# Kernel tuning notes

Measured on AMD Instinct MI355X. Metric: run time of the kernel, lower is better.

## Reference

```python
import jax, jax.numpy as jnp
import numpy as np

H, N, CH = 256, 64, 1

def _r2c(x):
    return x[..., 0] + 1j * x[..., 1]

def setup_inputs() -> dict:
    key = jax.random.key(0)
    kA, kB, kC, kdt = jax.random.split(key, 4)
    # Build a Hurwitz A (skew-Hermitian - 0.5*I) so dA = (I-dt/2 A)^-1 (I+dt/2 A) has spectral radius < 1
    M = jax.random.normal(kA, (H, N, N, 2), dtype=jnp.float32) / np.float32(np.sqrt(N))
    Mc = _r2c(M)
    Ac = 0.5 * (Mc - jnp.conjugate(jnp.swapaxes(Mc, -1, -2))) - 0.5 * jnp.eye(N, dtype=Mc.dtype)
    A = jnp.stack([Ac.real, Ac.imag], axis=-1)  # (H,N,N,2)
    B = jax.random.normal(kB, (H, N, 2), dtype=jnp.float32)
    C = jax.random.normal(kC, (CH, H, N, 2), dtype=jnp.float32)
    # log_dt uniform in [log(1e-3), log(1e-1)], shape (H,1) per bilinear docstring
    log_dt = jax.random.uniform(kdt, (H, 1), dtype=jnp.float32,
                                minval=np.float32(np.log(1e-3)), maxval=np.float32(np.log(1e-1)))
    return {"A": A, "B": B, "C": C, "log_dt": log_dt, "L": 2048}

def _bilinear(dt, Ac, Bc):
    # dt: (H,1), Ac: (H,N,N) complex, Bc: (H,N) complex
    n = Ac.shape[-1]
    I = jnp.eye(n, dtype=Ac.dtype)
    half = (dt.astype(Ac.real.dtype) / 2)[:, None]  # (H,1,1)
    A_back = I - half * Ac
    A_fwd = I + half * Ac
    dB = dt.astype(Ac.dtype) * jnp.linalg.solve(A_back, Bc[..., None])[..., 0]  # (H,N)
    dA = jnp.linalg.solve(A_back, A_fwd)  # (H,N,N)
    return dA, dB

def _krylov(L, dA, dB):
    # x[..., l] = dA^l dB via squaring-doubling, matches S4 krylov math
    x = dB[..., None]  # (H,N,1)
    A_ = dA
    while x.shape[-1] < L:
        x = jnp.concatenate([x, jnp.einsum('hnm,hml->hnl', A_, x)], axis=-1)
        A_ = A_ @ A_
    return x[..., :L]

def reference(A, B, C, log_dt, L):
    Ac, Bc, Cc = _r2c(A), _r2c(B), _r2c(C)
    dt = jnp.exp(log_dt)  # (H,1)
    dA, dB = _bilinear(dt, Ac, Bc)
    x = _krylov(L, dA, dB)  # (H,N,L) complex
    # k[c,h,l] = sum_n C[c,h,n] * (dA^l dB)[h,n]; torch .float() on complex keeps real part
    k = jnp.einsum('chn,hnl->chl', Cc, x).real.astype(jnp.float32)
    return k
```

## Files before the change

kernel.cpp:

```cpp
#include <hip/hip_runtime.h>
#include <math.h>

#define NH   256
#define NN   64
#define LSEQ 2048
#define SDW  68
#define NTH  1024

typedef __attribute__((ext_vector_type(8))) short short8;
typedef __attribute__((ext_vector_type(4))) float float4_t;

#define MFMA(a,b,c) __builtin_amdgcn_mfma_f32_16x16x32_bf16((a),(b),(c),0,0,0)
#define PERM_HI 0x07060302u
#define PERM_LO 0x05040100u

static __device__ __forceinline__ unsigned pack2(float v) {
    unsigned hv = __float_as_uint(v) & 0xffff0000u;
    float lo = v - __uint_as_float(hv);
    return __builtin_amdgcn_perm(hv, __float_as_uint(lo), PERM_HI);
}
static __device__ __forceinline__ float unpack2(unsigned w) {
    return __uint_as_float(w & 0xffff0000u) + __uint_as_float(w << 16);
}

static __device__ __forceinline__ void frag_vals(const unsigned* e, short8& hi, short8& lo) {
    unsigned lb[8];
#pragma unroll
    for (int m = 0; m < 8; ++m) {
        unsigned hv = e[m] & 0xffff0000u;
        lb[m] = __float_as_uint(__uint_as_float(e[m]) - __uint_as_float(hv));
    }
    union { short8 s; unsigned u[4]; } H, L;
#pragma unroll
    for (int m = 0; m < 4; ++m) {
        H.u[m] = __builtin_amdgcn_perm(e[2*m+1],  e[2*m],  PERM_HI);
        L.u[m] = __builtin_amdgcn_perm(lb[2*m+1], lb[2*m], PERM_HI);
    }
    hi = H.s; lo = L.s;
}
static __device__ __forceinline__ void frag_f32(const float* p, short8& hi, short8& lo) {
    const uint4* q = (const uint4*)p;
    uint4 d0 = q[0], d1 = q[1];
    unsigned e[8] = {d0.x, d0.y, d0.z, d0.w, d1.x, d1.y, d1.z, d1.w};
    frag_vals(e, hi, lo);
}
static __device__ __forceinline__ void frag_packed(const unsigned* p, short8& hi, short8& lo) {
    const uint4* q = (const uint4*)p;
    uint4 d0 = q[0], d1 = q[1];
    unsigned e[8] = {d0.x, d0.y, d0.z, d0.w, d1.x, d1.y, d1.z, d1.w};
    union { short8 s; unsigned u[4]; } H, L;
#pragma unroll
    for (int m = 0; m < 4; ++m) {
        H.u[m] = __builtin_amdgcn_perm(e[2*m+1], e[2*m], PERM_HI);
        L.u[m] = __builtin_amdgcn_perm(e[2*m+1], e[2*m], PERM_LO);
    }
    hi = H.s; lo = L.s;
}
static __device__ __forceinline__ short8 neg8(short8 v) {
    union { short8 s; int i[4]; } u; u.s = v;
#pragma unroll
    for (int m = 0; m < 4; ++m) u.i[m] ^= 0x80008000;
    return u.s;
}

template<bool AP, bool BP, bool IMAG>
static __device__ __forceinline__ void cmm_tile(
    const void* Ar_, const void* Ai_, const void* Br_, const void* Bi_,
    int arow, int bcol, int fq, float4_t& accR, float4_t& accI)
{
#pragma unroll
    for (int ks = 0; ks < 2; ++ks) {
        const int k0 = ks*32 + fq*8;
        short8 Arh, Arl, Aih, Ail, Brh, Brl, Bih, Bil;
        if (AP) {
            frag_packed((const unsigned*)Ar_ + arow*SDW + k0, Arh, Arl);
            frag_packed((const unsigned*)Ai_ + arow*SDW + k0, Aih, Ail);
        } else {
            frag_f32((const float*)Ar_ + arow*SDW + k0, Arh, Arl);
            frag_f32((const float*)Ai_ + arow*SDW + k0, Aih, Ail);
        }
        if (BP) {
            frag_packed((const unsigned*)Br_ + bcol*SDW + k0, Brh, Brl);
            frag_packed((const unsigned*)Bi_ + bcol*SDW + k0, Bih, Bil);
        } else {
            frag_f32((const float*)Br_ + bcol*SDW + k0, Brh, Brl);
            frag_f32((const float*)Bi_ + bcol*SDW + k0, Bih, Bil);
        }
        short8 nAih = neg8(Aih), nAil = neg8(Ail);
        accR = MFMA(Arh, Brh, accR); accR = MFMA(Arh, Brl, accR); accR = MFMA(Arl, Brh, accR);
        accR = MFMA(nAih, Bih, accR); accR = MFMA(nAih, Bil, accR); accR = MFMA(nAil, Bih, accR);
        if (IMAG) {
            accI = MFMA(Arh, Bih, accI); accI = MFMA(Arh, Bil, accI); accI = MFMA(Arl, Bih, accI);
            accI = MFMA(Aih, Brh, accI); accI = MFMA(Aih, Brl, accI); accI = MFMA(Ail, Brh, accI);
        }
    }
}

__global__ __launch_bounds__(NTH, 4) void ssm_kernel(
    const float* __restrict__ Ag,
    const float* __restrict__ Bg,
    const float* __restrict__ Cg,
    const float* __restrict__ LogDt,
    float* __restrict__ outp)
{
    __shared__ __align__(16) unsigned char lds[122880];
    unsigned* XRr = (unsigned*)(lds +      0);
    unsigned* XRi = (unsigned*)(lds +  17408);
    unsigned* XTr = (unsigned*)(lds +  34816);
    unsigned* XTi = (unsigned*)(lds +  52224);
    float*    Xfr = (float*)(lds +  69632);
    float*    Xfi = (float*)(lds +  87040);
    unsigned* U0u = (unsigned*)Xfr;
    unsigned* U1u = (unsigned*)Xfi;
    float*    Grf = (float*)(lds + 104448);
    float*    Gif = (float*)(lds + 113152);
    float*    bvr = (float*)(lds + 121856);
    float*    bvi = (float*)(lds + 122112);
    float*    urr = (float*)(lds + 122368);
    float*    uri = (float*)(lds + 122624);

    const int t    = threadIdx.x;
    const int lane = t & 63;
    const int wv   = t >> 6;
    const int ti   = wv >> 2, tj = wv & 3;
    const int fm   = lane & 15, fq = lane >> 4;
    const int h    = blockIdx.x;

    const float dt  = expf(LogDt[h]);
    const float hdt = 0.5f * dt;

    const float2* A2 = (const float2*)(Ag + (size_t)h * NN * NN * 2);
    const float4_t z4 = {0.f, 0.f, 0.f, 0.f};

#pragma unroll
    for (int e = 0; e < 4; ++e) {
        int idx = t + e*NTH;
        int i = idx >> 6, j = idx & 63;
        float2 a = A2[idx];
        unsigned pr = pack2((i == j ? 1.0f : 0.0f) + hdt * a.x);
        unsigned pi = pack2(hdt * a.y);
        XRr[i*SDW + j] = pr; XRi[i*SDW + j] = pi;
        XTr[j*SDW + i] = pr; XTi[j*SDW + i] = pi;
    }
    if (t < NN) {
        float2 bv = ((const float2*)Bg)[h*NN + t];
        float2 cv = ((const float2*)Cg)[h*NN + t];
        bvr[t] = bv.x; bvi[t] = bv.y;
        Grf[t] = cv.x; Gif[t] = cv.y;
    }
    __syncthreads();

    const int arow = ti*16 + fm;
    const int bcol = tj*16 + fm;

    {
        float4_t aR = z4, aI = z4;
#pragma unroll
        for (int ks = 0; ks < 2; ++ks) {
            const int k0 = ks*32 + fq*8;
            unsigned vr[8], vi[8];
#pragma unroll
            for (int j = 0; j < 8; ++j) {
                float2 a = A2[arow*NN + k0 + j];
                vr[j] = __float_as_uint((arow == k0 + j ? 1.0f : 0.0f) - hdt * a.x);
                vi[j] = __float_as_uint(-hdt * a.y);
            }
            short8 Arh, Arl, Aih, Ail, Brh, Brl, Bih, Bil;
            frag_vals(vr, Arh, Arl);
            frag_vals(vi, Aih, Ail);
            frag_packed(XTr + bcol*SDW + k0, Brh, Brl);
            frag_packed(XTi + bcol*SDW + k0, Bih, Bil);
            short8 nAih = neg8(Aih), nAil = neg8(Ail);
            aR = MFMA(Arh, Brh, aR); aR = MFMA(Arh, Brl, aR); aR = MFMA(Arl, Brh, aR);
            aR = MFMA(nAih, Bih, aR); aR = MFMA(nAih, Bil, aR); aR = MFMA(nAil, Bih, aR);
            aI = MFMA(Arh, Bih, aI); aI = MFMA(Arh, Bil, aI); aI = MFMA(Arl, Bih, aI);
            aI = MFMA(Aih, Brh, aI); aI = MFMA(Aih, Brl, aI); aI = MFMA(Ail, Brh, aI);
        }
#pragma unroll
        for (int rp = 0; rp < 2; ++rp) {
            int row0 = ti*16 + fq*4 + rp*2;
            uint2 wr; wr.x = pack2(aR[rp*2]); wr.y = pack2(aR[rp*2+1]);
            uint2 wi; wi.x = pack2(aI[rp*2]); wi.y = pack2(aI[rp*2+1]);
            *(uint2*)(U0u + bcol*SDW + row0) = wr;
            *(uint2*)(U1u + bcol*SDW + row0) = wi;
        }
    }
    __syncthreads();

    {
        float4_t aR = z4, aI = z4;
        cmm_tile<true, true, true>(XRr, XRi, U0u, U1u, arow, bcol, fq, aR, aI);
        __syncthreads();
#pragma unroll
        for (int r = 0; r < 4; ++r) {
            int row = ti*16 + fq*4 + r;
            XRr[row*SDW + bcol] = pack2(aR[r]);
            XRi[row*SDW + bcol] = pack2(aI[r]);
        }
    }
    __syncthreads();

    {
        float4_t aR = z4, aI = z4;
        cmm_tile<true, true, true>(XRr, XRi, U0u, U1u, arow, bcol, fq, aR, aI);
        float p_r[4], p_i[4];
#pragma unroll
        for (int r = 0; r < 4; ++r) {
            int row = ti*16 + fq*4 + r;
            float2 a = A2[row*NN + bcol];
            float dd  = (row == bcol ? 1.0f : 0.0f);
            float x1r = dd + hdt * a.x;
            float x1i = hdt * a.y;
            float vvr = unpack2(XRr[row*SDW + bcol]);
            float vvi = unpack2(XRi[row*SDW + bcol]);
            p_r[r] = 2.0f*(3.0f*x1r - 3.0f*vvr + aR[r]) - dd;
            p_i[r] = 2.0f*(3.0f*x1i - 3.0f*vvi + aI[r]);
        }
        __syncthreads();
        unsigned pr[4], pi[4];
#pragma unroll
        for (int r = 0; r < 4; ++r) {
            int row = ti*16 + fq*4 + r;
            pr[r] = pack2(p_r[r]); pi[r] = pack2(p_i[r]);
            XRr[row*SDW + bcol] = pr[r]; XRi[row*SDW + bcol] = pi[r];
        }
#pragma unroll
        for (int rp = 0; rp < 2; ++rp) {
            int row0 = ti*16 + fq*4 + rp*2;
            uint2 wr; wr.x = pr[rp*2]; wr.y = pr[rp*2+1];
            uint2 wi; wi.x = pi[rp*2]; wi.y = pi[rp*2+1];
            *(uint2*)(XTr + bcol*SDW + row0) = wr;
            *(uint2*)(XTi + bcol*SDW + row0) = wi;
        }
    }
    __syncthreads();

    {
        int n = t >> 4, part = t & 15;
        float ar = 0.f, ai = 0.f;
#pragma unroll
        for (int qq = 0; qq < 4; ++qq) {
            int k = part + 16*qq;
            float mr = unpack2(XRr[n*SDW + k]), mi = unpack2(XRi[n*SDW + k]);
            ar += mr*bvr[k] - mi*bvi[k];
            ai += mr*bvi[k] + mi*bvr[k];
        }
#pragma unroll
        for (int off = 8; off; off >>= 1) { ar += __shfl_xor(ar, off); ai += __shfl_xor(ai, off); }
        if (part == 0) { urr[n] = ar; uri[n] = ai; }
    }
    __syncthreads();

#pragma unroll 1
    for (int s = 1; s <= 9; ++s) {
        if (s == 1) {
            int n = t >> 4, part = t & 15;
            float ar = 0.f, ai = 0.f;
#pragma unroll
            for (int qq = 0; qq < 4; ++qq) {
                int k = part + 16*qq;
                float mr = unpack2(XRr[n*SDW + k]), mi = unpack2(XRi[n*SDW + k]);
                ar += mr*urr[k] - mi*uri[k];
                ai += mr*uri[k] + mi*urr[k];
            }
#pragma unroll
            for (int off = 8; off; off >>= 1) { ar += __shfl_xor(ar, off); ai += __shfl_xor(ai, off); }
            if (part == 0) {
                float u_r = urr[n], u_i = uri[n];
                Xfr[n]       = hdt*(u_r + bvr[n]);
                Xfi[n]       = hdt*(u_i + bvi[n]);
                Xfr[SDW + n] = hdt*(ar + u_r);
                Xfi[SDW + n] = hdt*(ai + u_i);
            }
        } else if (s <= 6) {
            const int C = 1 << (s-1);
            const int nT = (s == 6) ? 8 : 4;
            if (wv < nT) {
                const int rt = wv >> 2, ct = wv & 3;
                float4_t aR = z4, aI = z4;
                cmm_tile<false, true, true>(Xfr, Xfi, XRr, XRi, rt*16 + fm, ct*16 + fm, fq, aR, aI);
#pragma unroll
                for (int r = 0; r < 4; ++r) {
                    int row = rt*16 + fq*4 + r;
                    Xfr[(C+row)*SDW + ct*16 + fm] = aR[r];
                    Xfi[(C+row)*SDW + ct*16 + fm] = aI[r];
                }
            }
        } else {
            const int C = 1 << (s-7);
            if (wv < 4) {
                float4_t aR = z4, aI = z4;
                cmm_tile<false, true, true>(Grf, Gif, XTr, XTi, fm, wv*16 + fm, fq, aR, aI);
#pragma unroll
                for (int r = 0; r < 4; ++r) {
                    int row = C + fq*4 + r;
                    Grf[row*SDW + wv*16 + fm] = aR[r];
                    Gif[row*SDW + wv*16 + fm] = aI[r];
                }
            }
        }
        float4_t sR = z4, sI = z4;
        cmm_tile<true, true, true>(XRr, XRi, XTr, XTi, arow, bcol, fq, sR, sI);
        __syncthreads();
        unsigned pr[4], pi[4];
#pragma unroll
        for (int r = 0; r < 4; ++r) {
            int row = ti*16 + fq*4 + r;
            pr[r] = pack2(sR[r]); pi[r] = pack2(sI[r]);
            XRr[row*SDW + bcol] = pr[r]; XRi[row*SDW + bcol] = pi[r];
        }
#pragma unroll
        for (int rp = 0; rp < 2; ++rp) {
            int row0 = ti*16 + fq*4 + rp*2;
            uint2 wr; wr.x = pr[rp*2]; wr.y = pr[rp*2+1];
            uint2 wi; wi.x = pi[rp*2]; wi.y = pi[rp*2+1];
            *(uint2*)(XTr + bcol*SDW + row0) = wr;
            *(uint2*)(XTi + bcol*SDW + row0) = wi;
        }
        __syncthreads();
    }

#pragma unroll 1
    for (int tt = 0; tt < 4; ++tt) {
        if (tt < 3 && wv < 4) {
            const int ab = tt * 8;
            float4_t aR = z4, aI = z4;
            cmm_tile<false, true, true>(Grf, Gif, XTr, XTi, ab + fm, wv*16 + fm, fq, aR, aI);
#pragma unroll
            for (int r = 0; r < 4; ++r) {
                int orow = 8 + ab + fq*4 + r;
                if (orow < 32) {
                    Grf[orow*SDW + wv*16 + fm] = aR[r];
                    Gif[orow*SDW + wv*16 + fm] = aI[r];
                }
            }
        }
        if (wv >= 4 && wv < 8) {
            const int jb = tt * 8;
            float4_t aR = z4, aI = z4;
            cmm_tile<false, false, false>(Grf, Gif, Xfr, Xfi, jb + fm, (wv-4)*16 + fm, fq, aR, aI);
            if (fq < 2) {
                size_t base = (size_t)h * LSEQ;
#pragma unroll
                for (int r = 0; r < 4; ++r)
                    outp[base + (jb + fq*4 + r)*NN + (wv-4)*16 + fm] = aR[r];
            }
        }
        if (tt < 3) __syncthreads();
    }
}

extern "C" void kernel_launch(void* const* d_in, const int* in_sizes, int n_in,
                              void* d_out, int out_size, void* d_ws, size_t ws_size,
                              hipStream_t stream) {
    const float* A  = (const float*)d_in[0];
    const float* B  = (const float*)d_in[1];
    const float* C  = (const float*)d_in[2];
    const float* ld = (const float*)d_in[3];
    float* out = (float*)d_out;
    ssm_kernel<<<dim3(NH), dim3(NTH), 0, stream>>>(A, B, C, ld, out);
}
```

Before: 96.55 us.

## Store matrices as pre-split bf16 hi/lo planes and split complex accumulators

Replaces the packed hi/lo-in-one-word and fp32 shared-memory layouts with four separate bf16 planes (real hi, real lo, imag hi, imag lo) per matrix. MFMA fragments then load directly as short8 vectors with no perm or split work in the inner loop. The negation of the imaginary operand is dropped by accumulating the two real-part products in separate registers and subtracting at the end, and the imaginary part likewise uses two accumulators. This costs more accumulator registers, more LDS (about 127 KB) and more scattered 16-bit stores when writing results, and the fp32 buffers are now also held as split bf16.

```diff
diff --git a/kernel.cpp b/kernel.cpp
--- a/kernel.cpp
+++ b/kernel.cpp
@@ -4,23 +4,25 @@
 #define NH   256
 #define NN   64
 #define LSEQ 2048
-#define SDW  68
+#define RS   72
+#define PSZ  4608
+#define GSZ  2304
 #define NTH  1024
 
 typedef __attribute__((ext_vector_type(8))) short short8;
 typedef __attribute__((ext_vector_type(4))) float float4_t;
+typedef unsigned short u16;
 
 #define MFMA(a,b,c) __builtin_amdgcn_mfma_f32_16x16x32_bf16((a),(b),(c),0,0,0)
 #define PERM_HI 0x07060302u
-#define PERM_LO 0x05040100u
-
-static __device__ __forceinline__ unsigned pack2(float v) {
-    unsigned hv = __float_as_uint(v) & 0xffff0000u;
-    float lo = v - __uint_as_float(hv);
-    return __builtin_amdgcn_perm(hv, __float_as_uint(lo), PERM_HI);
-}
-static __device__ __forceinline__ float unpack2(unsigned w) {
-    return __uint_as_float(w & 0xffff0000u) + __uint_as_float(w << 16);
+
+static __device__ __forceinline__ void split2(float v, unsigned& hb, unsigned& lb) {
+    hb = __float_as_uint(v) & 0xffff0000u;
+    lb = __float_as_uint(v - __uint_as_float(hb));
+}
+static __device__ __forceinline__ float ld2(const u16* hp, const u16* lp, int idx) {
+    return __uint_as_float((unsigned)hp[idx] << 16)
+         + __uint_as_float((unsigned)lp[idx] << 16);
 }
 
 static __device__ __forceinline__ void frag_vals(const unsigned* e, short8& hi, short8& lo) {
@@ -38,62 +40,64 @@
     }
     hi = H.s; lo = L.s;
 }
-static __device__ __forceinline__ void frag_f32(const float* p, short8& hi, short8& lo) {
-    const uint4* q = (const uint4*)p;
-    uint4 d0 = q[0], d1 = q[1];
-    unsigned e[8] = {d0.x, d0.y, d0.z, d0.w, d1.x, d1.y, d1.z, d1.w};
-    frag_vals(e, hi, lo);
-}
-static __device__ __forceinline__ void frag_packed(const unsigned* p, short8& hi, short8& lo) {
-    const uint4* q = (const uint4*)p;
-    uint4 d0 = q[0], d1 = q[1];
-    unsigned e[8] = {d0.x, d0.y, d0.z, d0.w, d1.x, d1.y, d1.z, d1.w};
-    union { short8 s; unsigned u[4]; } H, L;
-#pragma unroll
-    for (int m = 0; m < 4; ++m) {
-        H.u[m] = __builtin_amdgcn_perm(e[2*m+1], e[2*m], PERM_HI);
-        L.u[m] = __builtin_amdgcn_perm(e[2*m+1], e[2*m], PERM_LO);
-    }
-    hi = H.s; lo = L.s;
-}
-static __device__ __forceinline__ short8 neg8(short8 v) {
-    union { short8 s; int i[4]; } u; u.s = v;
-#pragma unroll
-    for (int m = 0; m < 4; ++m) u.i[m] ^= 0x80008000;
-    return u.s;
-}
-
-template<bool AP, bool BP, bool IMAG>
+
+template<int ASZ, int BSZ, bool IMAG>
 static __device__ __forceinline__ void cmm_tile(
-    const void* Ar_, const void* Ai_, const void* Br_, const void* Bi_,
-    int arow, int bcol, int fq, float4_t& accR, float4_t& accI)
+    const u16* __restrict__ Ab, const u16* __restrict__ Bb,
+    int arow, int bcol, int fq,
+    float4_t& accP, float4_t& accN, float4_t& accI1, float4_t& accI2)
 {
 #pragma unroll
     for (int ks = 0; ks < 2; ++ks) {
         const int k0 = ks*32 + fq*8;
-        short8 Arh, Arl, Aih, Ail, Brh, Brl, Bih, Bil;
-        if (AP) {
-            frag_packed((const unsigned*)Ar_ + arow*SDW + k0, Arh, Arl);
-            frag_packed((const unsigned*)Ai_ + arow*SDW + k0, Aih, Ail);
-        } else {
-            frag_f32((const float*)Ar_ + arow*SDW + k0, Arh, Arl);
-            frag_f32((const float*)Ai_ + arow*SDW + k0, Aih, Ail);
-        }
-        if (BP) {
-            frag_packed((const unsigned*)Br_ + bcol*SDW + k0, Brh, Brl);
-            frag_packed((const unsigned*)Bi_ + bcol*SDW + k0, Bih, Bil);
-        } else {
-            frag_f32((const float*)Br_ + bcol*SDW + k0, Brh, Brl);
-            frag_f32((const float*)Bi_ + bcol*SDW + k0, Bih, Bil);
-        }
-        short8 nAih = neg8(Aih), nAil = neg8(Ail);
-        accR = MFMA(Arh, Brh, accR); accR = MFMA(Arh, Brl, accR); accR = MFMA(Arl, Brh, accR);
-        accR = MFMA(nAih, Bih, accR); accR = MFMA(nAih, Bil, accR); accR = MFMA(nAil, Bih, accR);
+        const u16* ap = Ab + arow*RS + k0;
+        const u16* bp = Bb + bcol*RS + k0;
+        short8 Arh = *(const short8*)(ap);
+        short8 Arl = *(const short8*)(ap + ASZ);
+        short8 Aih = *(const short8*)(ap + 2*ASZ);
+        short8 Ail = *(const short8*)(ap + 3*ASZ);
+        short8 Brh = *(const short8*)(bp);
+        short8 Brl = *(const short8*)(bp + BSZ);
+        short8 Bih = *(const short8*)(bp + 2*BSZ);
+        short8 Bil = *(const short8*)(bp + 3*BSZ);
+        accP = MFMA(Arh, Brh, accP); accP = MFMA(Arh, Brl, accP); accP = MFMA(Arl, Brh, accP);
+        accN = MFMA(Aih, Bih, accN); accN = MFMA(Aih, Bil, accN); accN = MFMA(Ail, Bih, accN);
         if (IMAG) {
-            accI = MFMA(Arh, Bih, accI); accI = MFMA(Arh, Bil, accI); accI = MFMA(Arl, Bih, accI);
-            accI = MFMA(Aih, Brh, accI); accI = MFMA(Aih, Brl, accI); accI = MFMA(Ail, Brh, accI);
-        }
-    }
+            accI1 = MFMA(Arh, Bih, accI1); accI1 = MFMA(Arh, Bil, accI1); accI1 = MFMA(Arl, Bih, accI1);
+            accI2 = MFMA(Aih, Brh, accI2); accI2 = MFMA(Aih, Brl, accI2); accI2 = MFMA(Ail, Brh, accI2);
+        }
+    }
+}
+
+static __device__ __forceinline__ void store_P_vals(
+    u16* XR, u16* XT, int ti, int bcol, int fq,
+    const float* p_r, const float* p_i)
+{
+    unsigned hR[4], lR[4], hI[4], lI[4];
+#pragma unroll
+    for (int r = 0; r < 4; ++r) {
+        split2(p_r[r], hR[r], lR[r]);
+        split2(p_i[r], hI[r], lI[r]);
+        int row = ti*16 + fq*4 + r;
+        XR[row*RS + bcol]         = (u16)(hR[r] >> 16);
+        XR[PSZ + row*RS + bcol]   = (u16)(lR[r] >> 16);
+        XR[2*PSZ + row*RS + bcol] = (u16)(hI[r] >> 16);
+        XR[3*PSZ + row*RS + bcol] = (u16)(lI[r] >> 16);
+    }
+    int tb = bcol*RS + ti*16 + fq*4;
+    uint2 w;
+    w.x = __builtin_amdgcn_perm(hR[1], hR[0], PERM_HI);
+    w.y = __builtin_amdgcn_perm(hR[3], hR[2], PERM_HI);
+    *(uint2*)&XT[tb] = w;
+    w.x = __builtin_amdgcn_perm(lR[1], lR[0], PERM_HI);
+    w.y = __builtin_amdgcn_perm(lR[3], lR[2], PERM_HI);
+    *(uint2*)&XT[PSZ + tb] = w;
+    w.x = __builtin_amdgcn_perm(hI[1], hI[0], PERM_HI);
+    w.y = __builtin_amdgcn_perm(hI[3], hI[2], PERM_HI);
+    *(uint2*)&XT[2*PSZ + tb] = w;
+    w.x = __builtin_amdgcn_perm(lI[1], lI[0], PERM_HI);
+    w.y = __builtin_amdgcn_perm(lI[3], lI[2], PERM_HI);
+    *(uint2*)&XT[3*PSZ + tb] = w;
 }
 
 __global__ __launch_bounds__(NTH, 4) void ssm_kernel(
@@ -103,21 +107,15 @@
     const float* __restrict__ LogDt,
     float* __restrict__ outp)
 {
-    __shared__ __align__(16) unsigned char lds[122880];
-    unsigned* XRr = (unsigned*)(lds +      0);
-    unsigned* XRi = (unsigned*)(lds +  17408);
-    unsigned* XTr = (unsigned*)(lds +  34816);
-    unsigned* XTi = (unsigned*)(lds +  52224);
-    float*    Xfr = (float*)(lds +  69632);
-    float*    Xfi = (float*)(lds +  87040);
-    unsigned* U0u = (unsigned*)Xfr;
-    unsigned* U1u = (unsigned*)Xfi;
-    float*    Grf = (float*)(lds + 104448);
-    float*    Gif = (float*)(lds + 113152);
-    float*    bvr = (float*)(lds + 121856);
-    float*    bvi = (float*)(lds + 122112);
-    float*    urr = (float*)(lds + 122368);
-    float*    uri = (float*)(lds + 122624);
+    __shared__ __align__(16) unsigned char lds[130048];
+    u16* XR = (u16*)(lds);
+    u16* XT = (u16*)(lds +  36864);
+    u16* XF = (u16*)(lds +  73728);
+    u16* Gm = (u16*)(lds + 110592);
+    float* bvr = (float*)(lds + 129024);
+    float* bvi = (float*)(lds + 129280);
+    float* urr = (float*)(lds + 129536);
+    float* uri = (float*)(lds + 129792);
 
     const int t    = threadIdx.x;
     const int lane = t & 63;
@@ -137,16 +135,29 @@
         int idx = t + e*NTH;
         int i = idx >> 6, j = idx & 63;
         float2 a = A2[idx];
-        unsigned pr = pack2((i == j ? 1.0f : 0.0f) + hdt * a.x);
-        unsigned pi = pack2(hdt * a.y);
-        XRr[i*SDW + j] = pr; XRi[i*SDW + j] = pi;
-        XTr[j*SDW + i] = pr; XTi[j*SDW + i] = pi;
+        unsigned hb, lb;
+        split2((i == j ? 1.0f : 0.0f) + hdt * a.x, hb, lb);
+        XR[i*RS + j]       = (u16)(hb >> 16);
+        XR[PSZ + i*RS + j] = (u16)(lb >> 16);
+        XT[j*RS + i]       = (u16)(hb >> 16);
+        XT[PSZ + j*RS + i] = (u16)(lb >> 16);
+        split2(hdt * a.y, hb, lb);
+        XR[2*PSZ + i*RS + j] = (u16)(hb >> 16);
+        XR[3*PSZ + i*RS + j] = (u16)(lb >> 16);
+        XT[2*PSZ + j*RS + i] = (u16)(hb >> 16);
+        XT[3*PSZ + j*RS + i] = (u16)(lb >> 16);
     }
     if (t < NN) {
         float2 bv = ((const float2*)Bg)[h*NN + t];
         float2 cv = ((const float2*)Cg)[h*NN + t];
         bvr[t] = bv.x; bvi[t] = bv.y;
-        Grf[t] = cv.x; Gif[t] = cv.y;
+        unsigned hb, lb;
+        split2(cv.x, hb, lb);
+        Gm[t]       = (u16)(hb >> 16);
+        Gm[GSZ + t] = (u16)(lb >> 16);
+        split2(cv.y, hb, lb);
+        Gm[2*GSZ + t] = (u16)(hb >> 16);
+        Gm[3*GSZ + t] = (u16)(lb >> 16);
     }
     __syncthreads();
 
@@ -154,7 +165,7 @@
     const int bcol = tj*16 + fm;
 
     {
-        float4_t aR = z4, aI = z4;
+        float4_t aP = z4, aN = z4, aI1 = z4, aI2 = z4;
 #pragma unroll
         for (int ks = 0; ks < 2; ++ks) {
             const int k0 = ks*32 + fq*8;
@@ -165,44 +176,56 @@
                 vr[j] = __float_as_uint((arow == k0 + j ? 1.0f : 0.0f) - hdt * a.x);
                 vi[j] = __float_as_uint(-hdt * a.y);
             }
-            short8 Arh, Arl, Aih, Ail, Brh, Brl, Bih, Bil;
+            short8 Arh, Arl, Aih, Ail;
             frag_vals(vr, Arh, Arl);
             frag_vals(vi, Aih, Ail);
-            frag_packed(XTr + bcol*SDW + k0, Brh, Brl);
-            frag_packed(XTi + bcol*SDW + k0, Bih, Bil);
-            short8 nAih = neg8(Aih), nAil = neg8(Ail);
-            aR = MFMA(Arh, Brh, aR); aR = MFMA(Arh, Brl, aR); aR = MFMA(Arl, Brh, aR);
-            aR = MFMA(nAih, Bih, aR); aR = MFMA(nAih, Bil, aR); aR = MFMA(nAil, Bih, aR);
-            aI = MFMA(Arh, Bih, aI); aI = MFMA(Arh, Bil, aI); aI = MFMA(Arl, Bih, aI);
-            aI = MFMA(Aih, Brh, aI); aI = MFMA(Aih, Brl, aI); aI = MFMA(Ail, Brh, aI);
+            const u16* bp = XT + bcol*RS + k0;
+            short8 Brh = *(const short8*)(bp);
+            short8 Brl = *(const short8*)(bp + PSZ);
+            short8 Bih = *(const short8*)(bp + 2*PSZ);
+            short8 Bil = *(const short8*)(bp + 3*PSZ);
+            aP = MFMA(Arh, Brh, aP); aP = MFMA(Arh, Brl, aP); aP = MFMA(Arl, Brh, aP);
+            aN = MFMA(Aih, Bih, aN); aN = MFMA(Aih, Bil, aN); aN = MFMA(Ail, Bih, aN);
+            aI1 = MFMA(Arh, Bih, aI1); aI1 = MFMA(Arh, Bil, aI1); aI1 = MFMA(Arl, Bih, aI1);
+            aI2 = MFMA(Aih, Brh, aI2); aI2 = MFMA(Aih, Brl, aI2); aI2 = MFMA(Ail, Brh, aI2);
         }
 #pragma unroll
         for (int rp = 0; rp < 2; ++rp) {
             int row0 = ti*16 + fq*4 + rp*2;
-            uint2 wr; wr.x = pack2(aR[rp*2]); wr.y = pack2(aR[rp*2+1]);
-            uint2 wi; wi.x = pack2(aI[rp*2]); wi.y = pack2(aI[rp*2+1]);
-            *(uint2*)(U0u + bcol*SDW + row0) = wr;
-            *(uint2*)(U1u + bcol*SDW + row0) = wi;
+            unsigned h0, l0, h1, l1;
+            split2(aP[rp*2]   - aN[rp*2],   h0, l0);
+            split2(aP[rp*2+1] - aN[rp*2+1], h1, l1);
+            *(unsigned*)&XF[bcol*RS + row0]       = __builtin_amdgcn_perm(h1, h0, PERM_HI);
+            *(unsigned*)&XF[PSZ + bcol*RS + row0] = __builtin_amdgcn_perm(l1, l0, PERM_HI);
+            split2(aI1[rp*2]   + aI2[rp*2],   h0, l0);
+            split2(aI1[rp*2+1] + aI2[rp*2+1], h1, l1);
+            *(unsigned*)&XF[2*PSZ + bcol*RS + row0] = __builtin_amdgcn_perm(h1, h0, PERM_HI);
+            *(unsigned*)&XF[3*PSZ + bcol*RS + row0] = __builtin_amdgcn_perm(l1, l0, PERM_HI);
         }
     }
     __syncthreads();
 
     {
-        float4_t aR = z4, aI = z4;
-        cmm_tile<true, true, true>(XRr, XRi, U0u, U1u, arow, bcol, fq, aR, aI);
+        float4_t aP = z4, aN = z4, aI1 = z4, aI2 = z4;
+        cmm_tile<PSZ, PSZ, true>(XR, XF, arow, bcol, fq, aP, aN, aI1, aI2);
         __syncthreads();
 #pragma unroll
         for (int r = 0; r < 4; ++r) {
             int row = ti*16 + fq*4 + r;
-            XRr[row*SDW + bcol] = pack2(aR[r]);
-            XRi[row*SDW + bcol] = pack2(aI[r]);
+            unsigned hb, lb;
+            split2(aP[r] - aN[r], hb, lb);
+            XR[row*RS + bcol]       = (u16)(hb >> 16);
+            XR[PSZ + row*RS + bcol] = (u16)(lb >> 16);
+            split2(aI1[r] + aI2[r], hb, lb);
+            XR[2*PSZ + row*RS + bcol] = (u16)(hb >> 16);
+            XR[3*PSZ + row*RS + bcol] = (u16)(lb >> 16);
         }
     }
     __syncthreads();
 
     {
-        float4_t aR = z4, aI = z4;
-        cmm_tile<true, true, true>(XRr, XRi, U0u, U1u, arow, bcol, fq, aR, aI);
+        float4_t aP = z4, aN = z4, aI1 = z4, aI2 = z4;
+        cmm_tile<PSZ, PSZ, true>(XR, XF, arow, bcol, fq, aP, aN, aI1, aI2);
         float p_r[4], p_i[4];
 #pragma unroll
         for (int r = 0; r < 4; ++r) {
@@ -211,27 +234,13 @@
             float dd  = (row == bcol ? 1.0f : 0.0f);
             float x1r = dd + hdt * a.x;
             float x1i = hdt * a.y;
-            float vvr = unpack2(XRr[row*SDW + bcol]);
-            float vvi = unpack2(XRi[row*SDW + bcol]);
-            p_r[r] = 2.0f*(3.0f*x1r - 3.0f*vvr + aR[r]) - dd;
-            p_i[r] = 2.0f*(3.0f*x1i - 3.0f*vvi + aI[r]);
+            float vvr = ld2(XR, XR + PSZ, row*RS + bcol);
+            float vvi = ld2(XR + 2*PSZ, XR + 3*PSZ, row*RS + bcol);
+            p_r[r] = 2.0f*(3.0f*x1r - 3.0f*vvr + (aP[r] - aN[r])) - dd;
+            p_i[r] = 2.0f*(3.0f*x1i - 3.0f*vvi + (aI1[r] + aI2[r]));
         }
         __syncthreads();
-        unsigned pr[4], pi[4];
-#pragma unroll
-        for (int r = 0; r < 4; ++r) {
-            int row = ti*16 + fq*4 + r;
-            pr[r] = pack2(p_r[r]); pi[r] = pack2(p_i[r]);
-            XRr[row*SDW + bcol] = pr[r]; XRi[row*SDW + bcol] = pi[r];
-        }
-#pragma unroll
-        for (int rp = 0; rp < 2; ++rp) {
-            int row0 = ti*16 + fq*4 + rp*2;
-            uint2 wr; wr.x = pr[rp*2]; wr.y = pr[rp*2+1];
-            uint2 wi; wi.x = pi[rp*2]; wi.y = pi[rp*2+1];
-            *(uint2*)(XTr + bcol*SDW + row0) = wr;
-            *(uint2*)(XTi + bcol*SDW + row0) = wi;
-        }
+        store_P_vals(XR, XT, ti, bcol, fq, p_r, p_i);
     }
     __syncthreads();
 
@@ -241,7 +250,8 @@
 #pragma unroll
         for (int qq = 0; qq < 4; ++qq) {
             int k = part + 16*qq;
-            float mr = unpack2(XRr[n*SDW + k]), mi = unpack2(XRi[n*SDW + k]);
+            float mr = ld2(XR, XR + PSZ, n*RS + k);
+            float mi = ld2(XR + 2*PSZ, XR + 3*PSZ, n*RS + k);
             ar += mr*bvr[k] - mi*bvi[k];
             ai += mr*bvi[k] + mi*bvr[k];
         }
@@ -259,7 +269,8 @@
 #pragma unroll
             for (int qq = 0; qq < 4; ++qq) {
                 int k = part + 16*qq;
-                float mr = unpack2(XRr[n*SDW + k]), mi = unpack2(XRi[n*SDW + k]);
+                float mr = ld2(XR, XR + PSZ, n*RS + k);
+                float mi = ld2(XR + 2*PSZ, XR + 3*PSZ, n*RS + k);
                 ar += mr*urr[k] - mi*uri[k];
                 ai += mr*uri[k] + mi*urr[k];
             }
@@ -267,56 +278,62 @@
             for (int off = 8; off; off >>= 1) { ar += __shfl_xor(ar, off); ai += __shfl_xor(ai, off); }
             if (part == 0) {
                 float u_r = urr[n], u_i = uri[n];
-                Xfr[n]       = hdt*(u_r + bvr[n]);
-                Xfi[n]       = hdt*(u_i + bvi[n]);
-                Xfr[SDW + n] = hdt*(ar + u_r);
-                Xfi[SDW + n] = hdt*(ai + u_i);
+                unsigned hb, lb;
+                split2(hdt*(u_r + bvr[n]), hb, lb);
+                XF[n]       = (u16)(hb >> 16); XF[PSZ + n]       = (u16)(lb >> 16);
+                split2(hdt*(u_i + bvi[n]), hb, lb);
+                XF[2*PSZ + n] = (u16)(hb >> 16); XF[3*PSZ + n]   = (u16)(lb >> 16);
+                split2(hdt*(ar + u_r), hb, lb);
+                XF[RS + n]       = (u16)(hb >> 16); XF[PSZ + RS + n]   = (u16)(lb >> 16);
+                split2(hdt*(ai + u_i), hb, lb);
+                XF[2*PSZ + RS + n] = (u16)(hb >> 16); XF[3*PSZ + RS + n] = (u16)(lb >> 16);
             }
         } else if (s <= 6) {
             const int C = 1 << (s-1);
             const int nT = (s == 6) ? 8 : 4;
             if (wv < nT) {
                 const int rt = wv >> 2, ct = wv & 3;
-                float4_t aR = z4, aI = z4;
-                cmm_tile<false, true, true>(Xfr, Xfi, XRr, XRi, rt*16 + fm, ct*16 + fm, fq, aR, aI);
+                float4_t aP = z4, aN = z4, aI1 = z4, aI2 = z4;
+                cmm_tile<PSZ, PSZ, true>(XF, XR, rt*16 + fm, ct*16 + fm, fq, aP, aN, aI1, aI2);
 #pragma unroll
                 for (int r = 0; r < 4; ++r) {
-                    int row = rt*16 + fq*4 + r;
-                    Xfr[(C+row)*SDW + ct*16 + fm] = aR[r];
-                    Xfi[(C+row)*SDW + ct*16 + fm] = aI[r];
+                    int orow = C + rt*16 + fq*4 + r;
+                    int oc   = ct*16 + fm;
+                    unsigned hb, lb;
+                    split2(aP[r] - aN[r], hb, lb);
+                    XF[orow*RS + oc]       = (u16)(hb >> 16);
+                    XF[PSZ + orow*RS + oc] = (u16)(lb >> 16);
+                    split2(aI1[r] + aI2[r], hb, lb);
+                    XF[2*PSZ + orow*RS + oc] = (u16)(hb >> 16);
+                    XF[3*PSZ + orow*RS + oc] = (u16)(lb >> 16);
                 }
             }
         } else {
             const int C = 1 << (s-7);
             if (wv < 4) {
-                float4_t aR = z4, aI = z4;
-                cmm_tile<false, true, true>(Grf, Gif, XTr, XTi, fm, wv*16 + fm, fq, aR, aI);
+                float4_t aP = z4, aN = z4, aI1 = z4, aI2 = z4;
+                cmm_tile<GSZ, PSZ, true>(Gm, XT, fm, wv*16 + fm, fq, aP, aN, aI1, aI2);
 #pragma unroll
                 for (int r = 0; r < 4; ++r) {
-                    int row = C + fq*4 + r;
-                    Grf[row*SDW + wv*16 + fm] = aR[r];
-                    Gif[row*SDW + wv*16 + fm] = aI[r];
+                    int orow = C + fq*4 + r;
+                    int oc   = wv*16 + fm;
+                    unsigned hb, lb;
+                    split2(aP[r] - aN[r], hb, lb);
+                    Gm[orow*RS + oc]       = (u16)(hb >> 16);
+                    Gm[GSZ + orow*RS + oc] = (u16)(lb >> 16);
+                    split2(aI1[r] + aI2[r], hb, lb);
+                    Gm[2*GSZ + orow*RS + oc] = (u16)(hb >> 16);
+                    Gm[3*GSZ + orow*RS + oc] = (u16)(lb >> 16);
                 }
             }
         }
-        float4_t sR = z4, sI = z4;
-        cmm_tile<true, true, true>(XRr, XRi, XTr, XTi, arow, bcol, fq, sR, sI);
+        float4_t sP = z4, sN = z4, sI1 = z4, sI2 = z4;
+        cmm_tile<PSZ, PSZ, true>(XR, XT, arow, bcol, fq, sP, sN, sI1, sI2);
         __syncthreads();
-        unsigned pr[4], pi[4];
-#pragma unroll
-        for (int r = 0; r < 4; ++r) {
-            int row = ti*16 + fq*4 + r;
-            pr[r] = pack2(sR[r]); pi[r] = pack2(sI[r]);
-            XRr[row*SDW + bcol] = pr[r]; XRi[row*SDW + bcol] = pi[r];
-        }
-#pragma unroll
-        for (int rp = 0; rp < 2; ++rp) {
-            int row0 = ti*16 + fq*4 + rp*2;
-            uint2 wr; wr.x = pr[rp*2]; wr.y = pr[rp*2+1];
-            uint2 wi; wi.x = pi[rp*2]; wi.y = pi[rp*2+1];
-            *(uint2*)(XTr + bcol*SDW + row0) = wr;
-            *(uint2*)(XTi + bcol*SDW + row0) = wi;
-        }
+        float p_r[4], p_i[4];
+#pragma unroll
+        for (int r = 0; r < 4; ++r) { p_r[r] = sP[r] - sN[r]; p_i[r] = sI1[r] + sI2[r]; }
+        store_P_vals(XR, XT, ti, bcol, fq, p_r, p_i);
         __syncthreads();
     }
 
@@ -324,26 +341,33 @@
     for (int tt = 0; tt < 4; ++tt) {
         if (tt < 3 && wv < 4) {
             const int ab = tt * 8;
-            float4_t aR = z4, aI = z4;
-            cmm_tile<false, true, true>(Grf, Gif, XTr, XTi, ab + fm, wv*16 + fm, fq, aR, aI);
+            float4_t aP = z4, aN = z4, aI1 = z4, aI2 = z4;
+            cmm_tile<GSZ, PSZ, true>(Gm, XT, ab + fm, wv*16 + fm, fq, aP, aN, aI1, aI2);
 #pragma unroll
             for (int r = 0; r < 4; ++r) {
                 int orow = 8 + ab + fq*4 + r;
                 if (orow < 32) {
-                    Grf[orow*SDW + wv*16 + fm] = aR[r];
-                    Gif[orow*SDW + wv*16 + fm] = aI[r];
+                    int oc = wv*16 + fm;
+                    unsigned hb, lb;
+                    split2(aP[r] - aN[r], hb, lb);
+                    Gm[orow*RS + oc]       = (u16)(hb >> 16);
+                    Gm[GSZ + orow*RS + oc] = (u16)(lb >> 16);
+                    split2(aI1[r] + aI2[r], hb, lb);
+                    Gm[2*GSZ + orow*RS + oc] = (u16)(hb >> 16);
+                    Gm[3*GSZ + orow*RS + oc] = (u16)(lb >> 16);
                 }
             }
         }
         if (wv >= 4 && wv < 8) {
             const int jb = tt * 8;
-            float4_t aR = z4, aI = z4;
-            cmm_tile<false, false, false>(Grf, Gif, Xfr, Xfi, jb + fm, (wv-4)*16 + fm, fq, aR, aI);
+            int ga = jb + fm; if (ga > 31) ga = 31;
+            float4_t aP = z4, aN = z4, aI1 = z4, aI2 = z4;
+            cmm_tile<GSZ, PSZ, false>(Gm, XF, ga, (wv-4)*16 + fm, fq, aP, aN, aI1, aI2);
             if (fq < 2) {
                 size_t base = (size_t)h * LSEQ;
 #pragma unroll
                 for (int r = 0; r < 4; ++r)
-                    outp[base + (jb + fq*4 + r)*NN + (wv-4)*16 + fm] = aR[r];
+                    outp[base + (jb + fq*4 + r)*NN + (wv-4)*16 + fm] = aP[r] - aN[r];
             }
         }
         if (tt < 3) __syncthreads();
```

Result: slower. 99.89 us (+3.5%).
